# Optimization experiments

Measured on AMD Instinct MI355X. Metric: run time of the kernel, lower is better.

The kernel has to match this reference:

```python
import jax, jax.numpy as jnp
import numpy as np

C = 8        # in_channels (forced: C//8 must be 1 for the broadcast matmul to work)
CQ = C // 8  # query/key channels = 1


def setup_inputs() -> dict:
    key = jax.random.key(0)
    ks = jax.random.split(key, 7)
    B, H, W = 16, 512, 512
    x = jax.random.normal(ks[0], (B, C, H, W), dtype=jnp.float32)
    # 1x1 conv weights stored as [out_ch, in_ch]
    sq = 1.0 / np.sqrt(C)
    Wq = jax.random.uniform(ks[1], (CQ, C), jnp.float32, -sq, sq)
    bq = jax.random.uniform(ks[2], (CQ,), jnp.float32, -sq, sq)
    Wk = jax.random.uniform(ks[3], (CQ, C), jnp.float32, -sq, sq)
    bk = jax.random.uniform(ks[4], (CQ,), jnp.float32, -sq, sq)
    Wv = jax.random.uniform(ks[5], (C, C), jnp.float32, -sq, sq)
    bv = jax.random.uniform(ks[6], (C,), jnp.float32, -sq, sq)
    return {"x": x, "Wq": Wq, "bq": bq, "Wk": Wk, "bk": bk, "Wv": Wv, "bv": bv}


def reference(x, Wq, bq, Wk, bk, Wv, bv):
    # 1x1 convs == per-pixel channel mixing
    q = jnp.einsum('bchw,oc->bohw', x, Wq) + bq[None, :, None, None]   # [B,1,H,W]
    k = jnp.einsum('bchw,oc->bohw', x, Wk) + bk[None, :, None, None]   # [B,1,H,W]
    v = jnp.einsum('bchw,oc->bohw', x, Wv) + bv[None, :, None, None]   # [B,C,H,W]
    # attention over rows: attn[b,o,i,j] = sum_w q[b,o,i,w] * k[b,o,j,w]  (no scaling, as in source)
    attn = jnp.einsum('boiw,bojw->boij', q, k)                          # [B,1,H,H]
    attn = jax.nn.softmax(attn, axis=-1)
    # broadcast matmul: [B,1,H,H] @ [B,C,H,W] -> [B,C,H,W]
    out = jnp.einsum('boij,bcjw->bciw', attn, v)
    return out
```

## Files before the change

### kernel.cpp

```cpp
#include <hip/hip_runtime.h>

constexpr int B = 16, C = 8, H = 512, W = 512;
constexpr int HW = H * W;

typedef short bf16x8 __attribute__((ext_vector_type(8)));
typedef float f32x4 __attribute__((ext_vector_type(4)));

__device__ __forceinline__ unsigned short f2bf(float f) {
    union { float f; unsigned u; } v; v.f = f;
    unsigned r = (v.u + 0x7FFFu + ((v.u >> 16) & 1u)) >> 16;
    return (unsigned short)r;
}
__device__ __forceinline__ float bf2f(unsigned short u) {
    union { unsigned u; float f; } v; v.u = (unsigned)u << 16;
    return v.f;
}
__device__ __forceinline__ void split1(float a, unsigned short& h, unsigned short& l) {
    h = f2bf(a);
    l = f2bf(a - bf2f(h));
}

__global__ __launch_bounds__(256) void qkv_fused_kernel(
    const float* __restrict__ x, const float* __restrict__ Wq, const float* __restrict__ bq,
    const float* __restrict__ Wk, const float* __restrict__ bk, const float* __restrict__ Wv,
    unsigned short* __restrict__ qh, unsigned short* __restrict__ ql,
    unsigned short* __restrict__ kh, unsigned short* __restrict__ kl,
    unsigned short* __restrict__ vt)
{
    __shared__ int ldsv[4][64][65];
    int b  = blockIdx.y;
    int j0 = (blockIdx.x >> 3) * 64;
    int w0 = (blockIdx.x & 7) * 64;
    const float* xb = x + (size_t)b * C * HW;
    int t  = threadIdx.x;
    int jr = t >> 4, c4 = (t & 15) * 4;

    float wq[8], wk[8], wv[8][8];
#pragma unroll
    for (int cc = 0; cc < 8; ++cc) {
        wq[cc] = Wq[cc]; wk[cc] = Wk[cc];
#pragma unroll
        for (int c = 0; c < 8; ++c) wv[c][cc] = Wv[c * 8 + cc];
    }
    float bq0 = bq[0], bk0 = bk[0];

#pragma unroll
    for (int rr = 0; rr < 4; ++rr) {
        int j = jr + rr * 16;
        size_t prow = (size_t)(j0 + j) * W + w0 + c4;
        float4 aq = make_float4(bq0, bq0, bq0, bq0);
        float4 ak = make_float4(bk0, bk0, bk0, bk0);
        float vacc[8][4] = {};
#pragma unroll
        for (int cc = 0; cc < 8; ++cc) {
            float4 xv = *reinterpret_cast<const float4*>(xb + (size_t)cc * HW + prow);
            aq.x = fmaf(wq[cc], xv.x, aq.x); aq.y = fmaf(wq[cc], xv.y, aq.y);
            aq.z = fmaf(wq[cc], xv.z, aq.z); aq.w = fmaf(wq[cc], xv.w, aq.w);
            ak.x = fmaf(wk[cc], xv.x, ak.x); ak.y = fmaf(wk[cc], xv.y, ak.y);
            ak.z = fmaf(wk[cc], xv.z, ak.z); ak.w = fmaf(wk[cc], xv.w, ak.w);
#pragma unroll
            for (int c = 0; c < 8; ++c) {
                vacc[c][0] = fmaf(wv[c][cc], xv.x, vacc[c][0]);
                vacc[c][1] = fmaf(wv[c][cc], xv.y, vacc[c][1]);
                vacc[c][2] = fmaf(wv[c][cc], xv.z, vacc[c][2]);
                vacc[c][3] = fmaf(wv[c][cc], xv.w, vacc[c][3]);
            }
        }
        size_t qoff = (size_t)b * HW + prow;
        ushort4 h4, l4;
        split1(aq.x, h4.x, l4.x); split1(aq.y, h4.y, l4.y);
        split1(aq.z, h4.z, l4.z); split1(aq.w, h4.w, l4.w);
        *reinterpret_cast<ushort4*>(qh + qoff) = h4;
        *reinterpret_cast<ushort4*>(ql + qoff) = l4;
        split1(ak.x, h4.x, l4.x); split1(ak.y, h4.y, l4.y);
        split1(ak.z, h4.z, l4.z); split1(ak.w, h4.w, l4.w);
        *reinterpret_cast<ushort4*>(kh + qoff) = h4;
        *reinterpret_cast<ushort4*>(kl + qoff) = l4;
#pragma unroll
        for (int cp = 0; cp < 4; ++cp)
#pragma unroll
            for (int i = 0; i < 4; ++i)
                ldsv[cp][j][c4 + i] =
                    (unsigned)f2bf(vacc[2 * cp][i]) | ((unsigned)f2bf(vacc[2 * cp + 1][i]) << 16);
    }
    __syncthreads();
#pragma unroll
    for (int cp = 0; cp < 4; ++cp) {
#pragma unroll
        for (int rr = 0; rr < 4; ++rr) {
            int w = jr + rr * 16;
            int d0 = ldsv[cp][c4 + 0][w];
            int d1 = ldsv[cp][c4 + 1][w];
            int d2 = ldsv[cp][c4 + 2][w];
            int d3 = ldsv[cp][c4 + 3][w];
            ushort4 e, o;
            e.x = (unsigned short)d0; o.x = (unsigned short)(d0 >> 16);
            e.y = (unsigned short)d1; o.y = (unsigned short)(d1 >> 16);
            e.z = (unsigned short)d2; o.z = (unsigned short)(d2 >> 16);
            e.w = (unsigned short)d3; o.w = (unsigned short)(d3 >> 16);
            size_t voff = (size_t)(w0 + w) * H + j0 + c4;
            *reinterpret_cast<ushort4*>(vt + ((size_t)(b * 8 + 2 * cp))     * HW + voff) = e;
            *reinterpret_cast<ushort4*>(vt + ((size_t)(b * 8 + 2 * cp + 1)) * HW + voff) = o;
        }
    }
}

__global__ __launch_bounds__(256, 2) void qk_mfma_kernel(
    const unsigned short* __restrict__ qh_, const unsigned short* __restrict__ ql_,
    const unsigned short* __restrict__ kh_, const unsigned short* __restrict__ kl_,
    float* __restrict__ attn)
{
    __shared__ char Ash[2][16384];
    __shared__ char Bsh[2][16384];
    int b  = blockIdx.z;
    int i0 = blockIdx.y * 128;
    int j0 = blockIdx.x * 128;
    int tid  = threadIdx.x;
    int lane = tid & 63, wv4 = tid >> 6;
    int wm = wv4 >> 1, wn = wv4 & 1;

    const char* qhB = (const char*)qh_ + (size_t)b * HW * 2;
    const char* qlB = (const char*)ql_ + (size_t)b * HW * 2;
    const char* khB = (const char*)kh_ + (size_t)b * HW * 2;
    const char* klB = (const char*)kl_ + (size_t)b * HW * 2;

    int ls  = (lane & 7) ^ (lane >> 3);
    int hsel = ls & 1, ssel = ls >> 1;

    f32x4 acc[4][4] = {};

#define STAGE(buf, kt)                                                                    \
    {                                                                                     \
        _Pragma("unroll")                                                                 \
        for (int pass = 0; pass < 4; ++pass) {                                            \
            int row = pass * 32 + wv4 * 8 + (lane >> 3);                                  \
            const char* sA = (hsel ? qlB : qhB) + (size_t)(i0 + row) * 1024 + (kt) * 64 + ssel * 16; \
            const char* sB = (hsel ? klB : khB) + (size_t)(j0 + row) * 1024 + (kt) * 64 + ssel * 16; \
            __builtin_amdgcn_global_load_lds(                                             \
                (const __attribute__((address_space(1))) unsigned int*)sA,                \
                (__attribute__((address_space(3))) unsigned int*)(Ash[buf] + pass * 4096 + wv4 * 1024), \
                16, 0, 0);                                                                \
            __builtin_amdgcn_global_load_lds(                                             \
                (const __attribute__((address_space(1))) unsigned int*)sB,                \
                (__attribute__((address_space(3))) unsigned int*)(Bsh[buf] + pass * 4096 + wv4 * 1024), \
                16, 0, 0);                                                                \
        }                                                                                 \
    }

    STAGE(0, 0);
    int cur = 0;
    for (int kt = 0; kt < 16; ++kt) {
        __syncthreads();
        if (kt + 1 < 16) STAGE(cur ^ 1, kt + 1);

        const char* Ab = Ash[cur];
        const char* Bb = Bsh[cur];
        bf16x8 ah[4], al[4], bh[4], bl[4];
        int sr = lane >> 4;
#pragma unroll
        for (int m = 0; m < 4; ++m) {
            int row = wm * 64 + m * 16 + (lane & 15);
            int sw = row & 7;
            ah[m] = *reinterpret_cast<const bf16x8*>(Ab + row * 128 + ((2 * sr)     ^ sw) * 16);
            al[m] = *reinterpret_cast<const bf16x8*>(Ab + row * 128 + ((2 * sr + 1) ^ sw) * 16);
        }
#pragma unroll
        for (int n = 0; n < 4; ++n) {
            int row = wn * 64 + n * 16 + (lane & 15);
            int sw = row & 7;
            bh[n] = *reinterpret_cast<const bf16x8*>(Bb + row * 128 + ((2 * sr)     ^ sw) * 16);
            bl[n] = *reinterpret_cast<const bf16x8*>(Bb + row * 128 + ((2 * sr + 1) ^ sw) * 16);
        }
#pragma unroll
        for (int m = 0; m < 4; ++m)
#pragma unroll
            for (int n = 0; n < 4; ++n) {
                acc[m][n] = __builtin_amdgcn_mfma_f32_16x16x32_bf16(ah[m], bh[n], acc[m][n], 0, 0, 0);
                acc[m][n] = __builtin_amdgcn_mfma_f32_16x16x32_bf16(ah[m], bl[n], acc[m][n], 0, 0, 0);
                acc[m][n] = __builtin_amdgcn_mfma_f32_16x16x32_bf16(al[m], bh[n], acc[m][n], 0, 0, 0);
            }
        cur ^= 1;
    }
#undef STAGE

    float* Cb = attn + (size_t)b * H * H;
#pragma unroll
    for (int m = 0; m < 4; ++m) {
        int i = i0 + wm * 64 + m * 16 + ((lane >> 4) << 2);
#pragma unroll
        for (int n = 0; n < 4; ++n) {
            int j = j0 + wn * 64 + n * 16 + (lane & 15);
#pragma unroll
            for (int r = 0; r < 4; ++r)
                Cb[(size_t)(i + r) * H + j] = acc[m][n][r];
        }
    }
}

__global__ __launch_bounds__(256) void softmax_kernel(
    const float* __restrict__ attn, unsigned short* __restrict__ attn_bf)
{
    int gid  = blockIdx.x * 256 + threadIdx.x;
    int row  = gid >> 6;
    int lane = gid & 63;
    const float* rp = attn + (size_t)row * H;
    float4 v0 = *reinterpret_cast<const float4*>(&rp[lane * 8]);
    float4 v1 = *reinterpret_cast<const float4*>(&rp[lane * 8 + 4]);
    float m = fmaxf(fmaxf(fmaxf(v0.x, v0.y), fmaxf(v0.z, v0.w)),
                    fmaxf(fmaxf(v1.x, v1.y), fmaxf(v1.z, v1.w)));
#pragma unroll
    for (int off = 32; off > 0; off >>= 1) m = fmaxf(m, __shfl_xor(m, off, 64));
    v0.x = __expf(v0.x - m); v0.y = __expf(v0.y - m);
    v0.z = __expf(v0.z - m); v0.w = __expf(v0.w - m);
    v1.x = __expf(v1.x - m); v1.y = __expf(v1.y - m);
    v1.z = __expf(v1.z - m); v1.w = __expf(v1.w - m);
    float s = v0.x + v0.y + v0.z + v0.w + v1.x + v1.y + v1.z + v1.w;
#pragma unroll
    for (int off = 32; off > 0; off >>= 1) s += __shfl_xor(s, off, 64);
    float inv = 1.0f / s;
    unsigned short* bp = attn_bf + (size_t)row * H + lane * 8;
    ushort4 o0, o1;
    o0.x = f2bf(v0.x * inv); o0.y = f2bf(v0.y * inv);
    o0.z = f2bf(v0.z * inv); o0.w = f2bf(v0.w * inv);
    o1.x = f2bf(v1.x * inv); o1.y = f2bf(v1.y * inv);
    o1.z = f2bf(v1.z * inv); o1.w = f2bf(v1.w * inv);
    *reinterpret_cast<ushort4*>(bp)     = o0;
    *reinterpret_cast<ushort4*>(bp + 4) = o1;
}

__global__ __launch_bounds__(256, 2) void pv_mfma_kernel(
    const unsigned short* __restrict__ attn_bf,
    const unsigned short* __restrict__ vt,
    const float* __restrict__ bv, float* __restrict__ out)
{
    __shared__ char Ash[2][128 * 128];
    __shared__ char Bsh[2][128 * 128];

    int b  = blockIdx.z;
    int i0 = blockIdx.y * 128;
    int n0 = blockIdx.x * 128;
    int tid  = threadIdx.x;
    int lane = tid & 63, wv = tid >> 6;
    int wm = wv >> 1, wn = wv & 1;

    const char* Abase = (const char*)(attn_bf + (size_t)b * H * H);
    const char* Bbase = (const char*)(vt + (size_t)b * C * HW + (size_t)n0 * H);

    int rsub = lane >> 3;
    int slot = lane & 7;
    int swsl = (slot ^ rsub) << 4;

    f32x4 acc[4][4] = {};

#define STAGE(buf, kt)                                                                   \
    {                                                                                    \
        int koff = (kt) * 128;                                                           \
        _Pragma("unroll")                                                                \
        for (int qq = 0; qq < 4; ++qq) {                                                 \
            int chunk = wv * 4 + qq;                                                     \
            int r = chunk * 8 + rsub;                                                    \
            __builtin_amdgcn_global_load_lds(                                            \
                (const __attribute__((address_space(1))) unsigned int*)                  \
                    (Abase + (size_t)(i0 + r) * 1024 + koff + swsl),                     \
                (__attribute__((address_space(3))) unsigned int*)(Ash[buf] + chunk * 1024), \
                16, 0, 0);                                                               \
            __builtin_amdgcn_global_load_lds(                                            \
                (const __attribute__((address_space(1))) unsigned int*)                  \
                    (Bbase + (size_t)r * 1024 + koff + swsl),                            \
                (__attribute__((address_space(3))) unsigned int*)(Bsh[buf] + chunk * 1024), \
                16, 0, 0);                                                               \
        }                                                                                \
    }

    STAGE(0, 0);
    int cur = 0;
    for (int kt = 0; kt < 8; ++kt) {
        __syncthreads();
        if (kt + 1 < 8) STAGE(cur ^ 1, kt + 1);

        const char* Ab = Ash[cur];
        const char* Bb = Bsh[cur];
        bf16x8 af[4][2], bf[4][2];
#pragma unroll
        for (int m = 0; m < 4; ++m) {
            int row = wm * 64 + m * 16 + (lane & 15);
            int base = row * 128 + ((lane >> 4) << 4);
            int sw = (row & 7) << 4;
            af[m][0] = *reinterpret_cast<const bf16x8*>(Ab + ((base)      ^ sw));
            af[m][1] = *reinterpret_cast<const bf16x8*>(Ab + ((base + 64) ^ sw));
        }
#pragma unroll
        for (int n = 0; n < 4; ++n) {
            int row = wn * 64 + n * 16 + (lane & 15);
            int base = row * 128 + ((lane >> 4) << 4);
            int sw = (row & 7) << 4;
            bf[n][0] = *reinterpret_cast<const bf16x8*>(Bb + ((base)      ^ sw));
            bf[n][1] = *reinterpret_cast<const bf16x8*>(Bb + ((base + 64) ^ sw));
        }
#pragma unroll
        for (int ks = 0; ks < 2; ++ks)
#pragma unroll
            for (int m = 0; m < 4; ++m)
#pragma unroll
                for (int n = 0; n < 4; ++n)
                    acc[m][n] = __builtin_amdgcn_mfma_f32_16x16x32_bf16(
                        af[m][ks], bf[n][ks], acc[m][n], 0, 0, 0);
        cur ^= 1;
    }
#undef STAGE

    int cc = n0 >> 9;
    int w0 = n0 & 511;
    float bias = bv[cc];
    float* outb = out + ((size_t)(b * C + cc)) * HW;
#pragma unroll
    for (int m = 0; m < 4; ++m) {
        int i = i0 + wm * 64 + m * 16 + ((lane >> 4) << 2);
#pragma unroll
        for (int n = 0; n < 4; ++n) {
            int w = w0 + wn * 64 + n * 16 + (lane & 15);
#pragma unroll
            for (int r = 0; r < 4; ++r)
                outb[(size_t)(i + r) * W + w] = acc[m][n][r] + bias;
        }
    }
}

extern "C" void kernel_launch(void* const* d_in, const int* in_sizes, int n_in,
                              void* d_out, int out_size, void* d_ws, size_t ws_size,
                              hipStream_t stream) {
    const float* x  = (const float*)d_in[0];
    const float* Wq = (const float*)d_in[1];
    const float* bq = (const float*)d_in[2];
    const float* Wk = (const float*)d_in[3];
    const float* bk = (const float*)d_in[4];
    const float* Wv = (const float*)d_in[5];
    const float* bv = (const float*)d_in[6];
    float* out = (float*)d_out;

    unsigned short* qh = (unsigned short*)d_ws;
    unsigned short* ql = qh + (size_t)B * HW;
    unsigned short* kh = ql + (size_t)B * HW;
    unsigned short* kl = kh + (size_t)B * HW;
    float* attnf = (float*)(kl + (size_t)B * HW);
    unsigned short* attnb = (unsigned short*)(attnf + (size_t)B * H * H);
    unsigned short* vtb = attnb + (size_t)B * H * H;

    qkv_fused_kernel<<<dim3(64, B), 256, 0, stream>>>(x, Wq, bq, Wk, bk, Wv, qh, ql, kh, kl, vtb);
    qk_mfma_kernel<<<dim3(4, 4, B), 256, 0, stream>>>(qh, ql, kh, kl, attnf);
    softmax_kernel<<<(B * H * 64) / 256, 256, 0, stream>>>(attnf, attnb);
    pv_mfma_kernel<<<dim3(32, 4, B), 256, 0, stream>>>(attnb, vtb, bv, out);
}
```

Measured before the change: 325.3 us.

## Remap blocks XCD-aware and halve PV K-tile for higher occupancy

Both MFMA kernels switch to a 1D grid with a swizzled block index, so blocks sharing the same batch (and, in PV, the same attention rows) land on the same XCD (lin&7) to improve L2 reuse. The PV kernel also halves its K-step from 128 to 64 bf16, cutting LDS from 64KB to 32KB per block, and raises the launch bound to 3 blocks per CU, with a new swizzle pattern to match. This trades more loop iterations and barriers for better occupancy and cache locality.

```diff
diff --git a/kernel.cpp b/kernel.cpp
--- a/kernel.cpp
+++ b/kernel.cpp
@@ -112,9 +112,12 @@
 {
     __shared__ char Ash[2][16384];
     __shared__ char Bsh[2][16384];
-    int b  = blockIdx.z;
-    int i0 = blockIdx.y * 128;
-    int j0 = blockIdx.x * 128;
+    int lin = blockIdx.x;
+    int swz = (lin & 7) * 32 + (lin >> 3);
+    int b   = swz >> 4;
+    int rr_ = swz & 15;
+    int i0 = (rr_ >> 2) * 128;
+    int j0 = (rr_ & 3) * 128;
     int tid  = threadIdx.x;
     int lane = tid & 63, wv4 = tid >> 6;
     int wm = wv4 >> 1, wn = wv4 & 1;
@@ -228,17 +231,20 @@
     *reinterpret_cast<ushort4*>(bp + 4) = o1;
 }
 
-__global__ __launch_bounds__(256, 2) void pv_mfma_kernel(
+__global__ __launch_bounds__(256, 3) void pv_mfma_kernel(
     const unsigned short* __restrict__ attn_bf,
     const unsigned short* __restrict__ vt,
     const float* __restrict__ bv, float* __restrict__ out)
 {
-    __shared__ char Ash[2][128 * 128];
-    __shared__ char Bsh[2][128 * 128];
-
-    int b  = blockIdx.z;
-    int i0 = blockIdx.y * 128;
-    int n0 = blockIdx.x * 128;
+    __shared__ char Ash[2][8192];
+    __shared__ char Bsh[2][8192];
+
+    int lin = blockIdx.x;
+    int swz = (lin & 7) * 256 + (lin >> 3);
+    int b   = swz >> 7;
+    int r_  = swz & 127;
+    int n0  = (r_ >> 2) * 128;
+    int i0  = (r_ & 3) * 128;
     int tid  = threadIdx.x;
     int lane = tid & 63, wv = tid >> 6;
     int wm = wv >> 1, wn = wv & 1;
@@ -246,27 +252,26 @@
     const char* Abase = (const char*)(attn_bf + (size_t)b * H * H);
     const char* Bbase = (const char*)(vt + (size_t)b * C * HW + (size_t)n0 * H);
 
-    int rsub = lane >> 3;
-    int slot = lane & 7;
-    int swsl = (slot ^ rsub) << 4;
+    int srow  = lane >> 2;
+    int sslot = ((lane & 3) ^ ((lane >> 3) & 3)) << 4;
 
     f32x4 acc[4][4] = {};
 
 #define STAGE(buf, kt)                                                                   \
     {                                                                                    \
-        int koff = (kt) * 128;                                                           \
+        int koff = (kt) * 64;                                                            \
         _Pragma("unroll")                                                                \
-        for (int qq = 0; qq < 4; ++qq) {                                                 \
-            int chunk = wv * 4 + qq;                                                     \
-            int r = chunk * 8 + rsub;                                                    \
+        for (int qq = 0; qq < 2; ++qq) {                                                 \
+            int chunk = wv * 2 + qq;                                                     \
+            int r = chunk * 16 + srow;                                                   \
             __builtin_amdgcn_global_load_lds(                                            \
                 (const __attribute__((address_space(1))) unsigned int*)                  \
-                    (Abase + (size_t)(i0 + r) * 1024 + koff + swsl),                     \
+                    (Abase + (size_t)(i0 + r) * 1024 + koff + sslot),                    \
                 (__attribute__((address_space(3))) unsigned int*)(Ash[buf] + chunk * 1024), \
                 16, 0, 0);                                                               \
             __builtin_amdgcn_global_load_lds(                                            \
                 (const __attribute__((address_space(1))) unsigned int*)                  \
-                    (Bbase + (size_t)r * 1024 + koff + swsl),                            \
+                    (Bbase + (size_t)r * 1024 + koff + sslot),                           \
                 (__attribute__((address_space(3))) unsigned int*)(Bsh[buf] + chunk * 1024), \
                 16, 0, 0);                                                               \
         }                                                                                \
@@ -274,37 +279,32 @@
 
     STAGE(0, 0);
     int cur = 0;
-    for (int kt = 0; kt < 8; ++kt) {
+    for (int kt = 0; kt < 16; ++kt) {
         __syncthreads();
-        if (kt + 1 < 8) STAGE(cur ^ 1, kt + 1);
+        if (kt + 1 < 16) STAGE(cur ^ 1, kt + 1);
 
         const char* Ab = Ash[cur];
         const char* Bb = Bsh[cur];
-        bf16x8 af[4][2], bf[4][2];
+        int kc = lane >> 4;
+        bf16x8 af[4], bf[4];
 #pragma unroll
         for (int m = 0; m < 4; ++m) {
             int row = wm * 64 + m * 16 + (lane & 15);
-            int base = row * 128 + ((lane >> 4) << 4);
-            int sw = (row & 7) << 4;
-            af[m][0] = *reinterpret_cast<const bf16x8*>(Ab + ((base)      ^ sw));
-            af[m][1] = *reinterpret_cast<const bf16x8*>(Ab + ((base + 64) ^ sw));
+            af[m] = *reinterpret_cast<const bf16x8*>(
+                Ab + row * 64 + ((kc ^ ((row >> 1) & 3)) << 4));
         }
 #pragma unroll
         for (int n = 0; n < 4; ++n) {
             int row = wn * 64 + n * 16 + (lane & 15);
-            int base = row * 128 + ((lane >> 4) << 4);
-            int sw = (row & 7) << 4;
-            bf[n][0] = *reinterpret_cast<const bf16x8*>(Bb + ((base)      ^ sw));
-            bf[n][1] = *reinterpret_cast<const bf16x8*>(Bb + ((base + 64) ^ sw));
-        }
-#pragma unroll
-        for (int ks = 0; ks < 2; ++ks)
-#pragma unroll
-            for (int m = 0; m < 4; ++m)
-#pragma unroll
-                for (int n = 0; n < 4; ++n)
-                    acc[m][n] = __builtin_amdgcn_mfma_f32_16x16x32_bf16(
-                        af[m][ks], bf[n][ks], acc[m][n], 0, 0, 0);
+            bf[n] = *reinterpret_cast<const bf16x8*>(
+                Bb + row * 64 + ((kc ^ ((row >> 1) & 3)) << 4));
+        }
+#pragma unroll
+        for (int m = 0; m < 4; ++m)
+#pragma unroll
+            for (int n = 0; n < 4; ++n)
+                acc[m][n] = __builtin_amdgcn_mfma_f32_16x16x32_bf16(
+                    af[m], bf[n], acc[m][n], 0, 0, 0);
         cur ^= 1;
     }
 #undef STAGE
@@ -347,7 +347,7 @@
     unsigned short* vtb = attnb + (size_t)B * H * H;
 
     qkv_fused_kernel<<<dim3(64, B), 256, 0, stream>>>(x, Wq, bq, Wk, bk, Wv, qh, ql, kh, kl, vtb);
-    qk_mfma_kernel<<<dim3(4, 4, B), 256, 0, stream>>>(qh, ql, kh, kl, attnf);
+    qk_mfma_kernel<<<256, 256, 0, stream>>>(qh, ql, kh, kl, attnf);
     softmax_kernel<<<(B * H * 64) / 256, 256, 0, stream>>>(attnf, attnb);
-    pv_mfma_kernel<<<dim3(32, 4, B), 256, 0, stream>>>(attnb, vtb, bv, out);
-}
+    pv_mfma_kernel<<<2048, 256, 0, stream>>>(attnb, vtb, bv, out);
+}
```

Measured after the change: 323.2 us. Within noise of the previous version (-0.7%).
